# Kernel optimization log

Hardware: AMD Instinct MI355X
Metric: run time of the kernel (lower is better)

The kernel has to match this reference:

```python
import jax, jax.numpy as jnp
import numpy as np

NUM_HEADS = 16
HEAD_DIM = 64
KERNEL = 13  # odd
DIM = NUM_HEADS * HEAD_DIM
SCALE = HEAD_DIM ** -0.5


def setup_inputs() -> dict:
    key = jax.random.key(0)
    ks = jax.random.split(key, 6)
    B, L = 4, 4096
    return {
        "x": jax.random.normal(ks[0], (B, L, DIM), jnp.float32),
        "w_qkv": jax.random.normal(ks[1], (DIM, 3 * DIM), jnp.float32) * 0.02,
        "b_qkv": jax.random.normal(ks[2], (3 * DIM,), jnp.float32) * 0.02,
        "rpb": jax.random.normal(ks[3], (NUM_HEADS, 2 * KERNEL - 1), jnp.float32) * 0.02,
        "w_proj": jax.random.normal(ks[4], (DIM, DIM), jnp.float32) * 0.02,
        "b_proj": jax.random.normal(ks[5], (DIM,), jnp.float32) * 0.02,
    }


def _na1d(q, k, v, rpb, kernel_size):
    # q,k,v: [B,H,L,D]; rpb: [H, 2K-1]. dilation == 1.
    L = q.shape[2]
    K = kernel_size
    r = K // 2
    i = jnp.arange(L)
    # neighborhood start, clamped so each query sees exactly K keys (NATTEN semantics)
    ni = jnp.clip(i - r, 0, L - K)                    # [L]
    nbr = ni[:, None] + jnp.arange(K)                 # [L,K] key indices
    k_nb = k[:, :, nbr]                               # [B,H,L,K,D]
    attn = jnp.einsum("bhld,bhlkd->bhlk", q, k_nb)   # windowed QK
    # relative-position-bias start index: bias idx = (key_pos - i) + (K-1)
    pi = ni - i + (K - 1)                             # [L]
    bias = rpb[:, pi[:, None] + jnp.arange(K)]        # [H,L,K]
    attn = jax.nn.softmax(attn + bias[None], axis=-1)
    v_nb = v[:, :, nbr]                               # [B,H,L,K,D]
    return jnp.einsum("bhlk,bhlkd->bhld", attn, v_nb)


def reference(x, w_qkv, b_qkv, rpb, w_proj, b_proj):
    B, L, C = x.shape
    qkv = x @ w_qkv + b_qkv                           # [B,L,3C]
    qkv = qkv.reshape(B, L, 3, NUM_HEADS, HEAD_DIM).transpose(2, 0, 3, 1, 4)
    q, k, v = qkv[0] * SCALE, qkv[1], qkv[2]          # [B,H,L,D]
    out = _na1d(q, k, v, rpb, KERNEL)                 # [B,H,L,D]
    out = out.transpose(0, 2, 1, 3).reshape(B, L, C)
    return out @ w_proj + b_proj
```

## Files before the change

### kernel.cpp

```cpp
#include <hip/hip_runtime.h>

typedef __bf16 bf16x8_t __attribute__((ext_vector_type(8)));
typedef float  f32x4_t  __attribute__((ext_vector_type(4)));
typedef float  floatx4  __attribute__((ext_vector_type(4)));
typedef unsigned short ushortx4 __attribute__((ext_vector_type(4)));

__device__ __forceinline__ float bf2f(unsigned short u) {
    union { unsigned int i; float f; } c; c.i = ((unsigned int)u) << 16; return c.f;
}
__device__ __forceinline__ unsigned short f2bf(float f) {
    union { float f; unsigned int i; } c; c.f = f;
    unsigned int u = c.i;
    u += 0x7fffu + ((u >> 16) & 1u);
    return (unsigned short)(u >> 16);
}
__device__ __forceinline__ void unpack8(uint4 u, float* dst, float sc) {
    dst[0] = bf2f((unsigned short)(u.x & 0xffff)) * sc;
    dst[1] = bf2f((unsigned short)(u.x >> 16)) * sc;
    dst[2] = bf2f((unsigned short)(u.y & 0xffff)) * sc;
    dst[3] = bf2f((unsigned short)(u.y >> 16)) * sc;
    dst[4] = bf2f((unsigned short)(u.z & 0xffff)) * sc;
    dst[5] = bf2f((unsigned short)(u.z >> 16)) * sc;
    dst[6] = bf2f((unsigned short)(u.w & 0xffff)) * sc;
    dst[7] = bf2f((unsigned short)(u.w >> 16)) * sc;
}

__device__ __forceinline__ void load_lds16(const unsigned short* g, unsigned short* l) {
    __builtin_amdgcn_global_load_lds(
        (const __attribute__((address_space(1))) unsigned int*)g,
        (__attribute__((address_space(3))) unsigned int*)l, 16, 0, 0);
}

__global__ __launch_bounds__(256) void convert_f32_bf16(
    const float* __restrict__ x, unsigned short* __restrict__ xb)
{
    size_t i = ((size_t)blockIdx.x * 256 + threadIdx.x) * 8;
    floatx4 a = *reinterpret_cast<const floatx4*>(x + i);
    floatx4 b = *reinterpret_cast<const floatx4*>(x + i + 4);
    uint4 o;
    o.x = (unsigned int)f2bf(a.x) | ((unsigned int)f2bf(a.y) << 16);
    o.y = (unsigned int)f2bf(a.z) | ((unsigned int)f2bf(a.w) << 16);
    o.z = (unsigned int)f2bf(b.x) | ((unsigned int)f2bf(b.y) << 16);
    o.w = (unsigned int)f2bf(b.z) | ((unsigned int)f2bf(b.w) << 16);
    *reinterpret_cast<uint4*>(xb + i) = o;
}

__global__ __launch_bounds__(256) void transpose_f32_to_bf16(
    const float* __restrict__ W, unsigned short* __restrict__ Wt,
    int Kdim, int Ndim)
{
    __shared__ float tile[32][33];
    const int n0 = blockIdx.x * 32, k0 = blockIdx.y * 32;
    const int tx = threadIdx.x & 31, ty = threadIdx.x >> 5;
#pragma unroll
    for (int r = 0; r < 4; ++r) {
        int k = ty + r * 8;
        tile[k][tx] = W[(size_t)(k0 + k) * Ndim + n0 + tx];
    }
    __syncthreads();
#pragma unroll
    for (int r = 0; r < 4; ++r) {
        int n = ty + r * 8;
        Wt[(size_t)(n0 + n) * Kdim + k0 + tx] = f2bf(tile[tx][n]);
    }
}

#define TBM 256
#define TBN 256
#define TBK 32

template<bool C_F32>
__global__ __launch_bounds__(512, 2) void gemm_pipe_kernel(
    const unsigned short* __restrict__ A, const unsigned short* __restrict__ Wt,
    const float* __restrict__ bias, void* __restrict__ Cp,
    int N, int K, int lda, int ldc)
{
    __shared__ __align__(16) unsigned short As[4][TBM * TBK];
    __shared__ __align__(16) unsigned short Bs[4][TBN * TBK];

    const int tid  = threadIdx.x;
    const int lane = tid & 63;
    const int wid  = tid >> 6;
    const int wm   = wid >> 2;
    const int wn   = wid & 3;
    const int quad = lane >> 4;
    const int lr   = lane & 15;

    const int gx  = gridDim.x;
    const int cpx = (gx * gridDim.y) >> 3;
    const int bid = blockIdx.y * gx + blockIdx.x;
    const int nid = (bid & 7) * cpx + (bid >> 3);
    const int m0 = (nid / gx) * TBM;
    const int n0 = (nid % gx) * TBN;

    const int s_row = tid >> 2;
    const int c_sw  = ((tid & 3) ^ ((tid >> 3) & 3)) * 8;
    const int xq    = (quad ^ ((lr >> 1) & 3)) * 8;
    const int NT    = K >> 5;

    const unsigned short* Ag  = A  + (size_t)(m0 + s_row) * lda + c_sw;
    const unsigned short* Ag2 = Ag + (size_t)128 * lda;
    const unsigned short* Bg  = Wt + (size_t)(n0 + s_row) * K + c_sw;
    const unsigned short* Bg2 = Bg + (size_t)128 * K;

    f32x4_t acc[8][4];
#pragma unroll
    for (int i = 0; i < 8; ++i)
#pragma unroll
        for (int j = 0; j < 4; ++j)
            acc[i][j] = (f32x4_t){0.f, 0.f, 0.f, 0.f};

#pragma unroll
    for (int tt = 0; tt < 3; ++tt) {
        load_lds16(Ag  + tt * TBK, &As[tt][wid * 512]);
        load_lds16(Ag2 + tt * TBK, &As[tt][4096 + wid * 512]);
        load_lds16(Bg  + tt * TBK, &Bs[tt][wid * 512]);
        load_lds16(Bg2 + tt * TBK, &Bs[tt][4096 + wid * 512]);
    }
    asm volatile("s_waitcnt vmcnt(8)" ::: "memory");
    __builtin_amdgcn_s_barrier();

    for (int tt = 0; tt < NT; ++tt) {
        const int b = tt & 3;
        const unsigned short* pa = &As[b][0];
        const unsigned short* pb = &Bs[b][0];
        const bool st = (tt + 3) < NT;
        const int  sb = (tt + 3) & 3;
        const int  ko = (tt + 3) * TBK;

        bf16x8_t a0 = *reinterpret_cast<const bf16x8_t*>(pa + (wm * 128 +   0 + lr) * TBK + xq);
        bf16x8_t a1 = *reinterpret_cast<const bf16x8_t*>(pa + (wm * 128 +  16 + lr) * TBK + xq);
        bf16x8_t a2 = *reinterpret_cast<const bf16x8_t*>(pa + (wm * 128 +  32 + lr) * TBK + xq);
        bf16x8_t a3 = *reinterpret_cast<const bf16x8_t*>(pa + (wm * 128 +  48 + lr) * TBK + xq);
        bf16x8_t bv[4];
#pragma unroll
        for (int j = 0; j < 4; ++j)
            bv[j] = *reinterpret_cast<const bf16x8_t*>(pb + (wn * 64 + j * 16 + lr) * TBK + xq);
        if (st) {
            load_lds16(Ag  + ko, &As[sb][wid * 512]);
            load_lds16(Ag2 + ko, &As[sb][4096 + wid * 512]);
        }
        __builtin_amdgcn_s_barrier();

        __builtin_amdgcn_s_setprio(1);
#pragma unroll
        for (int j = 0; j < 4; ++j) {
            acc[0][j] = __builtin_amdgcn_mfma_f32_16x16x32_bf16(a0, bv[j], acc[0][j], 0, 0, 0);
            acc[1][j] = __builtin_amdgcn_mfma_f32_16x16x32_bf16(a1, bv[j], acc[1][j], 0, 0, 0);
            acc[2][j] = __builtin_amdgcn_mfma_f32_16x16x32_bf16(a2, bv[j], acc[2][j], 0, 0, 0);
            acc[3][j] = __builtin_amdgcn_mfma_f32_16x16x32_bf16(a3, bv[j], acc[3][j], 0, 0, 0);
        }
        __builtin_amdgcn_s_setprio(0);

        bf16x8_t a4 = *reinterpret_cast<const bf16x8_t*>(pa + (wm * 128 +  64 + lr) * TBK + xq);
        bf16x8_t a5 = *reinterpret_cast<const bf16x8_t*>(pa + (wm * 128 +  80 + lr) * TBK + xq);
        bf16x8_t a6 = *reinterpret_cast<const bf16x8_t*>(pa + (wm * 128 +  96 + lr) * TBK + xq);
        bf16x8_t a7 = *reinterpret_cast<const bf16x8_t*>(pa + (wm * 128 + 112 + lr) * TBK + xq);
        if (st) {
            load_lds16(Bg  + ko, &Bs[sb][wid * 512]);
            load_lds16(Bg2 + ko, &Bs[sb][4096 + wid * 512]);
        }
        __builtin_amdgcn_s_barrier();

        __builtin_amdgcn_s_setprio(1);
#pragma unroll
        for (int j = 0; j < 4; ++j) {
            acc[4][j] = __builtin_amdgcn_mfma_f32_16x16x32_bf16(a4, bv[j], acc[4][j], 0, 0, 0);
            acc[5][j] = __builtin_amdgcn_mfma_f32_16x16x32_bf16(a5, bv[j], acc[5][j], 0, 0, 0);
            acc[6][j] = __builtin_amdgcn_mfma_f32_16x16x32_bf16(a6, bv[j], acc[6][j], 0, 0, 0);
            acc[7][j] = __builtin_amdgcn_mfma_f32_16x16x32_bf16(a7, bv[j], acc[7][j], 0, 0, 0);
        }
        __builtin_amdgcn_s_setprio(0);

        if (tt < NT - 3)       asm volatile("s_waitcnt vmcnt(8)" ::: "memory");
        else if (tt == NT - 3) asm volatile("s_waitcnt vmcnt(4)" ::: "memory");
        else                   asm volatile("s_waitcnt vmcnt(0)" ::: "memory");
        __builtin_amdgcn_s_barrier();
    }

#pragma unroll
    for (int j = 0; j < 4; ++j) {
        int col = n0 + wn * 64 + j * 16 + lr;
        float bj = bias[col];
#pragma unroll
        for (int i = 0; i < 8; ++i) {
            int rbase = m0 + wm * 128 + i * 16 + quad * 4;
#pragma unroll
            for (int r = 0; r < 4; ++r) {
                float v = acc[i][j][r] + bj;
                size_t idx = (size_t)(rbase + r) * ldc + col;
                if (C_F32) ((float*)Cp)[idx] = v;
                else       ((unsigned short*)Cp)[idx] = f2bf(v);
            }
        }
    }
}

#define BM 128
#define BN 128
#define BK 32
#define LDT 40

template<bool A_F32, bool C_F32, bool BT>
__global__ __launch_bounds__(256) void gemm_bias_kernel(
    const void* __restrict__ Ap, const void* __restrict__ Wp,
    const float* __restrict__ bias, void* __restrict__ Cp,
    int N, int K, int lda, int ldc)
{
    __shared__ __align__(16) unsigned short As[BM * LDT];
    __shared__ __align__(16) unsigned short Bs[BN * LDT];

    const int tid  = threadIdx.x;
    const int lane = tid & 63;
    const int wid  = tid >> 6;
    const int wm   = wid >> 1;
    const int wn   = wid & 1;
    const int quad = lane >> 4;
    const int lr   = lane & 15;

    const int m0 = blockIdx.y * BM;
    const int n0 = blockIdx.x * BN;

    f32x4_t acc[4][4];
#pragma unroll
    for (int i = 0; i < 4; ++i)
#pragma unroll
        for (int j = 0; j < 4; ++j)
            acc[i][j] = (f32x4_t){0.f, 0.f, 0.f, 0.f};

    for (int k0 = 0; k0 < K; k0 += BK) {
        if (A_F32) {
            const float* A = (const float*)Ap;
#pragma unroll
            for (int it = 0; it < 4; ++it) {
                int q   = tid + it * 256;
                int row = q >> 3;
                int col = (q & 7) * 4;
                floatx4 f = *reinterpret_cast<const floatx4*>(A + (size_t)(m0 + row) * lda + k0 + col);
                ushortx4 s;
                s.x = f2bf(f.x); s.y = f2bf(f.y); s.z = f2bf(f.z); s.w = f2bf(f.w);
                *reinterpret_cast<ushortx4*>(&As[row * LDT + col]) = s;
            }
        } else {
            const unsigned short* A = (const unsigned short*)Ap;
            int a_row = tid >> 2;
            int a_col = (tid & 3) * 8;
#pragma unroll
            for (int r = 0; r < 2; ++r) {
                int row = a_row + r * 64;
                uint4 u = *reinterpret_cast<const uint4*>(A + (size_t)(m0 + row) * lda + k0 + a_col);
                *reinterpret_cast<uint4*>(&As[row * LDT + a_col]) = u;
            }
        }
        if (BT) {
            const unsigned short* Wt = (const unsigned short*)Wp;
            int b_row = tid >> 2;
            int b_col = (tid & 3) * 8;
#pragma unroll
            for (int r = 0; r < 2; ++r) {
                int n = b_row + r * 64;
                uint4 u = *reinterpret_cast<const uint4*>(Wt + (size_t)(n0 + n) * K + k0 + b_col);
                *reinterpret_cast<uint4*>(&Bs[n * LDT + b_col]) = u;
            }
        } else {
            const float* W = (const float*)Wp;
#pragma unroll
            for (int it = 0; it < 4; ++it) {
                int q  = tid + it * 256;
                int kk = q >> 5;
                int nn = (q & 31) * 4;
                floatx4 f = *reinterpret_cast<const floatx4*>(W + (size_t)(k0 + kk) * N + n0 + nn);
                Bs[(nn + 0) * LDT + kk] = f2bf(f.x);
                Bs[(nn + 1) * LDT + kk] = f2bf(f.y);
                Bs[(nn + 2) * LDT + kk] = f2bf(f.z);
                Bs[(nn + 3) * LDT + kk] = f2bf(f.w);
            }
        }
        __syncthreads();

        bf16x8_t av[4], bv[4];
#pragma unroll
        for (int i = 0; i < 4; ++i)
            av[i] = *reinterpret_cast<const bf16x8_t*>(&As[(wm * 64 + i * 16 + lr) * LDT + quad * 8]);
#pragma unroll
        for (int j = 0; j < 4; ++j)
            bv[j] = *reinterpret_cast<const bf16x8_t*>(&Bs[(wn * 64 + j * 16 + lr) * LDT + quad * 8]);

#pragma unroll
        for (int i = 0; i < 4; ++i)
#pragma unroll
            for (int j = 0; j < 4; ++j)
                acc[i][j] = __builtin_amdgcn_mfma_f32_16x16x32_bf16(av[i], bv[j], acc[i][j], 0, 0, 0);

        __syncthreads();
    }

#pragma unroll
    for (int j = 0; j < 4; ++j) {
        int col = n0 + wn * 64 + j * 16 + lr;
        float bj = bias[col];
#pragma unroll
        for (int i = 0; i < 4; ++i) {
            int rbase = m0 + wm * 64 + i * 16 + quad * 4;
#pragma unroll
            for (int r = 0; r < 4; ++r) {
                float v = acc[i][j][r] + bj;
                size_t idx = (size_t)(rbase + r) * ldc + col;
                if (C_F32) ((float*)Cp)[idx] = v;
                else       ((unsigned short*)Cp)[idx] = f2bf(v);
            }
        }
    }
}

#define NA_L 4096
#define NA_K 13
#define NA_H 16
#define NA_D 64
#define NA_SCALE 0.125f
#define TL  64
#define WIN 76
#define KD  68

__global__ __launch_bounds__(256) void na1d_tiled_kernel(
    unsigned short* qkv, const float* __restrict__ rpb)
{
    __shared__ __align__(16) float ks[WIN * KD];
    __shared__ __align__(16) float vs[WIN * KD];
    __shared__ __align__(16) float qs[TL * KD];
    __shared__ float wgt[TL][NA_K];

    const int bid = blockIdx.x;
    const int h  = bid & 15;
    const int lt = (bid >> 4) & 63;
    const int b  = bid >> 10;
    const int l0 = lt * TL;
    const int rs = l0 - 6;

    const int t = threadIdx.x;
    const size_t rowbase = (size_t)b * NA_L;

    {
        const int qr = t >> 2;
        const int qc = (t & 3) * 16;
        const unsigned short* qsrc = qkv + (rowbase + l0 + qr) * 3072 + h * 64 + qc;
        uint4 q0 = *reinterpret_cast<const uint4*>(qsrc);
        uint4 q1 = *reinterpret_cast<const uint4*>(qsrc + 8);

        const int r0 = t >> 3;
        const int cc = (t & 7) * 8;
        int g0 = rs + r0;      g0 = g0 < 0 ? 0 : (g0 > NA_L - 1 ? NA_L - 1 : g0);
        int g1 = rs + r0 + 32; g1 = g1 < 0 ? 0 : (g1 > NA_L - 1 ? NA_L - 1 : g1);
        const unsigned short* p0 = qkv + (rowbase + g0) * 3072 + 1024 + h * 64 + cc;
        const unsigned short* p1 = qkv + (rowbase + g1) * 3072 + 1024 + h * 64 + cc;
        uint4 k0 = *reinterpret_cast<const uint4*>(p0);
        uint4 v0 = *reinterpret_cast<const uint4*>(p0 + 1024);
        uint4 k1 = *reinterpret_cast<const uint4*>(p1);
        uint4 v1 = *reinterpret_cast<const uint4*>(p1 + 1024);
        uint4 k2, v2;
        if (t < 96) {
            int g2 = rs + r0 + 64; g2 = g2 < 0 ? 0 : (g2 > NA_L - 1 ? NA_L - 1 : g2);
            const unsigned short* p2 = qkv + (rowbase + g2) * 3072 + 1024 + h * 64 + cc;
            k2 = *reinterpret_cast<const uint4*>(p2);
            v2 = *reinterpret_cast<const uint4*>(p2 + 1024);
        }

        unpack8(q0, &qs[qr * KD + qc], NA_SCALE);
        unpack8(q1, &qs[qr * KD + qc + 8], NA_SCALE);
        unpack8(k0, &ks[r0 * KD + cc], 1.f);
        unpack8(v0, &vs[r0 * KD + cc], 1.f);
        unpack8(k1, &ks[(r0 + 32) * KD + cc], 1.f);
        unpack8(v1, &vs[(r0 + 32) * KD + cc], 1.f);
        if (t < 96) {
            unpack8(k2, &ks[(r0 + 64) * KD + cc], 1.f);
            unpack8(v2, &vs[(r0 + 64) * KD + cc], 1.f);
        }
    }
    __syncthreads();

    {
        const int l  = t & 63;
        const int jb = (t >> 6) * 4;
        int ig = l0 + l;
        int ni = ig - 6;
        if (ni < 0) ni = 0;
        if (ni > NA_L - NA_K) ni = NA_L - NA_K;
        int rid = ni - rs;
        int pi  = ni - ig + 12;
        const floatx4* qr = reinterpret_cast<const floatx4*>(&qs[l * KD]);
        const floatx4* k0 = reinterpret_cast<const floatx4*>(&ks[(rid + jb + 0) * KD]);
        const floatx4* k1 = reinterpret_cast<const floatx4*>(&ks[(rid + jb + 1) * KD]);
        const floatx4* k2 = reinterpret_cast<const floatx4*>(&ks[(rid + jb + 2) * KD]);
        const floatx4* k3 = reinterpret_cast<const floatx4*>(&ks[(rid + jb + 3) * KD]);
        floatx4 a0 = {0,0,0,0}, a1 = {0,0,0,0}, a2 = {0,0,0,0}, a3 = {0,0,0,0};
#pragma unroll
        for (int c = 0; c < 16; ++c) {
            floatx4 qv = qr[c];
            a0 += qv * k0[c];
            a1 += qv * k1[c];
            a2 += qv * k2[c];
            a3 += qv * k3[c];
        }
        float s0 = a0.x + a0.y + a0.z + a0.w;
        float s1 = a1.x + a1.y + a1.z + a1.w;
        float s2 = a2.x + a2.y + a2.z + a2.w;
        float s3 = a3.x + a3.y + a3.z + a3.w;
        const float* rp = rpb + h * 25 + pi;
        if (jb + 0 < NA_K) wgt[l][jb + 0] = s0 + rp[jb + 0];
        if (jb + 1 < NA_K) wgt[l][jb + 1] = s1 + rp[jb + 1];
        if (jb + 2 < NA_K) wgt[l][jb + 2] = s2 + rp[jb + 2];
        if (jb + 3 < NA_K) wgt[l][jb + 3] = s3 + rp[jb + 3];
    }
    __syncthreads();

    if (t < TL) {
        float m = -1e30f;
#pragma unroll
        for (int j = 0; j < NA_K; ++j) m = fmaxf(m, wgt[t][j]);
        float sum = 0.f;
#pragma unroll
        for (int j = 0; j < NA_K; ++j) {
            float e = expf(wgt[t][j] - m);
            wgt[t][j] = e;
            sum += e;
        }
        float inv = 1.f / sum;
#pragma unroll
        for (int j = 0; j < NA_K; ++j) wgt[t][j] *= inv;
    }
    __syncthreads();

    {
        const int l  = t & 63;
        const int d0 = (t >> 6) * 16;
        int ig = l0 + l;
        int ni = ig - 6;
        if (ni < 0) ni = 0;
        if (ni > NA_L - NA_K) ni = NA_L - NA_K;
        int rid = ni - rs;
        floatx4 o0 = {0,0,0,0}, o1 = {0,0,0,0}, o2 = {0,0,0,0}, o3 = {0,0,0,0};
#pragma unroll
        for (int j = 0; j < NA_K; ++j) {
            float w = wgt[l][j];
            const floatx4* vr = reinterpret_cast<const floatx4*>(&vs[(rid + j) * KD + d0]);
            o0 += w * vr[0];
            o1 += w * vr[1];
            o2 += w * vr[2];
            o3 += w * vr[3];
        }
        unsigned short* dst = qkv + (rowbase + ig) * 3072 + h * 64 + d0;
        uint4 p0, p1;
        p0.x = (unsigned int)f2bf(o0.x) | ((unsigned int)f2bf(o0.y) << 16);
        p0.y = (unsigned int)f2bf(o0.z) | ((unsigned int)f2bf(o0.w) << 16);
        p0.z = (unsigned int)f2bf(o1.x) | ((unsigned int)f2bf(o1.y) << 16);
        p0.w = (unsigned int)f2bf(o1.z) | ((unsigned int)f2bf(o1.w) << 16);
        p1.x = (unsigned int)f2bf(o2.x) | ((unsigned int)f2bf(o2.y) << 16);
        p1.y = (unsigned int)f2bf(o2.z) | ((unsigned int)f2bf(o2.w) << 16);
        p1.z = (unsigned int)f2bf(o3.x) | ((unsigned int)f2bf(o3.y) << 16);
        p1.w = (unsigned int)f2bf(o3.z) | ((unsigned int)f2bf(o3.w) << 16);
        *reinterpret_cast<uint4*>(dst)     = p0;
        *reinterpret_cast<uint4*>(dst + 8) = p1;
    }
}

extern "C" void kernel_launch(void* const* d_in, const int* in_sizes, int n_in,
                              void* d_out, int out_size, void* d_ws, size_t ws_size,
                              hipStream_t stream)
{
    const float* x      = (const float*)d_in[0];
    const float* w_qkv  = (const float*)d_in[1];
    const float* b_qkv  = (const float*)d_in[2];
    const float* rpb    = (const float*)d_in[3];
    const float* w_proj = (const float*)d_in[4];
    const float* b_proj = (const float*)d_in[5];
    float* out = (float*)d_out;

    const int M  = 4 * 4096;
    const int K  = 1024;
    const int N1 = 3072;
    const int N2 = 1024;

    unsigned short* qkv = (unsigned short*)d_ws;
    unsigned short* Wt1 = qkv + (size_t)M * N1;
    unsigned short* Wt2 = Wt1 + (size_t)N1 * K;
    unsigned short* xb  = Wt2 + (size_t)N2 * K;
    size_t need_mid  = ((size_t)M * N1 + (size_t)N1 * K + (size_t)N2 * K) * 2;
    size_t need_fast = need_mid + (size_t)M * K * 2;

    const int na_grid = 4 * (NA_L / TL) * NA_H;

    if (ws_size >= need_fast) {
        convert_f32_bf16<<<dim3(M * K / (256 * 8)), 256, 0, stream>>>(x, xb);
        transpose_f32_to_bf16<<<dim3(N1 / 32, K / 32), 256, 0, stream>>>(w_qkv, Wt1, K, N1);
        transpose_f32_to_bf16<<<dim3(N2 / 32, K / 32), 256, 0, stream>>>(w_proj, Wt2, K, N2);
        gemm_pipe_kernel<false><<<dim3(N1 / TBN, M / TBM), 512, 0, stream>>>(
            xb, Wt1, b_qkv, qkv, N1, K, K, N1);
        na1d_tiled_kernel<<<dim3(na_grid), 256, 0, stream>>>(qkv, rpb);
        gemm_pipe_kernel<true><<<dim3(N2 / TBN, M / TBM), 512, 0, stream>>>(
            qkv, Wt2, b_proj, out, N2, K, N1, N2);
    } else if (ws_size >= need_mid) {
        transpose_f32_to_bf16<<<dim3(N1 / 32, K / 32), 256, 0, stream>>>(w_qkv, Wt1, K, N1);
        transpose_f32_to_bf16<<<dim3(N2 / 32, K / 32), 256, 0, stream>>>(w_proj, Wt2, K, N2);
        gemm_bias_kernel<true, false, true><<<dim3(N1 / BN, M / BM), 256, 0, stream>>>(
            x, Wt1, b_qkv, qkv, N1, K, K, N1);
        na1d_tiled_kernel<<<dim3(na_grid), 256, 0, stream>>>(qkv, rpb);
        gemm_bias_kernel<false, true, true><<<dim3(N2 / BN, M / BM), 256, 0, stream>>>(
            qkv, Wt2, b_proj, out, N2, K, N1, N2);
    } else {
        gemm_bias_kernel<true, false, false><<<dim3(N1 / BN, M / BM), 256, 0, stream>>>(
            x, w_qkv, b_qkv, qkv, N1, K, K, N1);
        na1d_tiled_kernel<<<dim3(na_grid), 256, 0, stream>>>(qkv, rpb);
        gemm_bias_kernel<false, true, false><<<dim3(N2 / BN, M / BM), 256, 0, stream>>>(
            qkv, w_proj, b_proj, out, N2, K, N1, N2);
    }
}
```

Baseline: 386.0 us.

## Merge GEMM main-loop halves under one barrier and stage bf16 epilogue through LDS

The pipelined 256x256 GEMM now keeps its A and B stages in one shared buffer. Each iteration issues all four prefetch loads up front, reads all eight A fragments and four B fragments, then runs the 32 MFMAs under a single barrier instead of two half-iterations with two barriers. For bf16 outputs the epilogue writes biased results into a per-wave XOR-swizzled LDS tile, then writes them out as 16-byte row-contiguous global stores instead of scattered 2-byte stores. Holding all eight A fragments at once raises register pressure and gives less interleaving of LDS reads with MFMAs.

```diff
diff --git a/kernel.cpp b/kernel.cpp
--- a/kernel.cpp
+++ b/kernel.cpp
@@ -75,8 +75,7 @@
     const float* __restrict__ bias, void* __restrict__ Cp,
     int N, int K, int lda, int ldc)
 {
-    __shared__ __align__(16) unsigned short As[4][TBM * TBK];
-    __shared__ __align__(16) unsigned short Bs[4][TBN * TBK];
+    __shared__ __align__(16) unsigned short SMEM[8][8192];
 
     const int tid  = threadIdx.x;
     const int lane = tid & 63;
@@ -112,64 +111,43 @@
 
 #pragma unroll
     for (int tt = 0; tt < 3; ++tt) {
-        load_lds16(Ag  + tt * TBK, &As[tt][wid * 512]);
-        load_lds16(Ag2 + tt * TBK, &As[tt][4096 + wid * 512]);
-        load_lds16(Bg  + tt * TBK, &Bs[tt][wid * 512]);
-        load_lds16(Bg2 + tt * TBK, &Bs[tt][4096 + wid * 512]);
+        load_lds16(Ag  + tt * TBK, &SMEM[tt][wid * 512]);
+        load_lds16(Ag2 + tt * TBK, &SMEM[tt][4096 + wid * 512]);
+        load_lds16(Bg  + tt * TBK, &SMEM[4 + tt][wid * 512]);
+        load_lds16(Bg2 + tt * TBK, &SMEM[4 + tt][4096 + wid * 512]);
     }
     asm volatile("s_waitcnt vmcnt(8)" ::: "memory");
     __builtin_amdgcn_s_barrier();
 
     for (int tt = 0; tt < NT; ++tt) {
         const int b = tt & 3;
-        const unsigned short* pa = &As[b][0];
-        const unsigned short* pb = &Bs[b][0];
+        const unsigned short* pa = &SMEM[b][0];
+        const unsigned short* pb = &SMEM[4 + b][0];
         const bool st = (tt + 3) < NT;
         const int  sb = (tt + 3) & 3;
         const int  ko = (tt + 3) * TBK;
 
-        bf16x8_t a0 = *reinterpret_cast<const bf16x8_t*>(pa + (wm * 128 +   0 + lr) * TBK + xq);
-        bf16x8_t a1 = *reinterpret_cast<const bf16x8_t*>(pa + (wm * 128 +  16 + lr) * TBK + xq);
-        bf16x8_t a2 = *reinterpret_cast<const bf16x8_t*>(pa + (wm * 128 +  32 + lr) * TBK + xq);
-        bf16x8_t a3 = *reinterpret_cast<const bf16x8_t*>(pa + (wm * 128 +  48 + lr) * TBK + xq);
-        bf16x8_t bv[4];
+        if (st) {
+            load_lds16(Ag  + ko, &SMEM[sb][wid * 512]);
+            load_lds16(Ag2 + ko, &SMEM[sb][4096 + wid * 512]);
+            load_lds16(Bg  + ko, &SMEM[4 + sb][wid * 512]);
+            load_lds16(Bg2 + ko, &SMEM[4 + sb][4096 + wid * 512]);
+        }
+
+        bf16x8_t bv[4], av[8];
 #pragma unroll
         for (int j = 0; j < 4; ++j)
             bv[j] = *reinterpret_cast<const bf16x8_t*>(pb + (wn * 64 + j * 16 + lr) * TBK + xq);
-        if (st) {
-            load_lds16(Ag  + ko, &As[sb][wid * 512]);
-            load_lds16(Ag2 + ko, &As[sb][4096 + wid * 512]);
-        }
-        __builtin_amdgcn_s_barrier();
+#pragma unroll
+        for (int i = 0; i < 8; ++i)
+            av[i] = *reinterpret_cast<const bf16x8_t*>(pa + (wm * 128 + i * 16 + lr) * TBK + xq);
 
         __builtin_amdgcn_s_setprio(1);
 #pragma unroll
-        for (int j = 0; j < 4; ++j) {
-            acc[0][j] = __builtin_amdgcn_mfma_f32_16x16x32_bf16(a0, bv[j], acc[0][j], 0, 0, 0);
-            acc[1][j] = __builtin_amdgcn_mfma_f32_16x16x32_bf16(a1, bv[j], acc[1][j], 0, 0, 0);
-            acc[2][j] = __builtin_amdgcn_mfma_f32_16x16x32_bf16(a2, bv[j], acc[2][j], 0, 0, 0);
-            acc[3][j] = __builtin_amdgcn_mfma_f32_16x16x32_bf16(a3, bv[j], acc[3][j], 0, 0, 0);
-        }
-        __builtin_amdgcn_s_setprio(0);
-
-        bf16x8_t a4 = *reinterpret_cast<const bf16x8_t*>(pa + (wm * 128 +  64 + lr) * TBK + xq);
-        bf16x8_t a5 = *reinterpret_cast<const bf16x8_t*>(pa + (wm * 128 +  80 + lr) * TBK + xq);
-        bf16x8_t a6 = *reinterpret_cast<const bf16x8_t*>(pa + (wm * 128 +  96 + lr) * TBK + xq);
-        bf16x8_t a7 = *reinterpret_cast<const bf16x8_t*>(pa + (wm * 128 + 112 + lr) * TBK + xq);
-        if (st) {
-            load_lds16(Bg  + ko, &Bs[sb][wid * 512]);
-            load_lds16(Bg2 + ko, &Bs[sb][4096 + wid * 512]);
-        }
-        __builtin_amdgcn_s_barrier();
-
-        __builtin_amdgcn_s_setprio(1);
-#pragma unroll
-        for (int j = 0; j < 4; ++j) {
-            acc[4][j] = __builtin_amdgcn_mfma_f32_16x16x32_bf16(a4, bv[j], acc[4][j], 0, 0, 0);
-            acc[5][j] = __builtin_amdgcn_mfma_f32_16x16x32_bf16(a5, bv[j], acc[5][j], 0, 0, 0);
-            acc[6][j] = __builtin_amdgcn_mfma_f32_16x16x32_bf16(a6, bv[j], acc[6][j], 0, 0, 0);
-            acc[7][j] = __builtin_amdgcn_mfma_f32_16x16x32_bf16(a7, bv[j], acc[7][j], 0, 0, 0);
-        }
+        for (int i = 0; i < 8; ++i)
+#pragma unroll
+            for (int j = 0; j < 4; ++j)
+                acc[i][j] = __builtin_amdgcn_mfma_f32_16x16x32_bf16(av[i], bv[j], acc[i][j], 0, 0, 0);
         __builtin_amdgcn_s_setprio(0);
 
         if (tt < NT - 3)       asm volatile("s_waitcnt vmcnt(8)" ::: "memory");
@@ -178,20 +156,46 @@
         __builtin_amdgcn_s_barrier();
     }
 
-#pragma unroll
-    for (int j = 0; j < 4; ++j) {
-        int col = n0 + wn * 64 + j * 16 + lr;
-        float bj = bias[col];
-#pragma unroll
-        for (int i = 0; i < 8; ++i) {
-            int rbase = m0 + wm * 128 + i * 16 + quad * 4;
-#pragma unroll
-            for (int r = 0; r < 4; ++r) {
-                float v = acc[i][j][r] + bj;
-                size_t idx = (size_t)(rbase + r) * ldc + col;
-                if (C_F32) ((float*)Cp)[idx] = v;
-                else       ((unsigned short*)Cp)[idx] = f2bf(v);
-            }
+    if (C_F32) {
+#pragma unroll
+        for (int j = 0; j < 4; ++j) {
+            int col = n0 + wn * 64 + j * 16 + lr;
+            float bj = bias[col];
+#pragma unroll
+            for (int i = 0; i < 8; ++i) {
+                int rbase = m0 + wm * 128 + i * 16 + quad * 4;
+#pragma unroll
+                for (int r = 0; r < 4; ++r) {
+                    float v = acc[i][j][r] + bj;
+                    ((float*)Cp)[(size_t)(rbase + r) * ldc + col] = v;
+                }
+            }
+        }
+    } else {
+        unsigned short* ep = &SMEM[wid][0];
+#pragma unroll
+        for (int j = 0; j < 4; ++j) {
+            float bj = bias[n0 + wn * 64 + j * 16 + lr];
+#pragma unroll
+            for (int i = 0; i < 8; ++i) {
+#pragma unroll
+                for (int r = 0; r < 4; ++r) {
+                    int row = i * 16 + quad * 4 + r;
+                    int col = j * 16 + lr;
+                    int ch  = (col >> 3) ^ (row & 7);
+                    ep[row * 64 + ch * 8 + (col & 7)] = f2bf(acc[i][j][r] + bj);
+                }
+            }
+        }
+        unsigned short* Cb = (unsigned short*)Cp;
+        const int cch = lane & 7;
+#pragma unroll
+        for (int s = 0; s < 16; ++s) {
+            int row = s * 8 + (lane >> 3);
+            int ch  = cch ^ (row & 7);
+            uint4 v = *reinterpret_cast<const uint4*>(&ep[row * 64 + ch * 8]);
+            *reinterpret_cast<uint4*>(
+                Cb + (size_t)(m0 + wm * 128 + row) * ldc + n0 + wn * 64 + cch * 8) = v;
         }
     }
 }
```

Measured after the change: 366.3 us. 5.1% less time.
